# Performance work log

Measured on AMD Instinct MI355X. Metric: run time of the kernel, lower is better.

## Reference

```python
import jax, jax.numpy as jnp
import numpy as np

EPS = 1e-12  # F.normalize default eps

def _unfold3(x):
    # torch F.unfold(kernel=(3,3), padding=1): [B,C,H,W] -> [B, C*9, H*W]
    # channel-major, kernel offsets row-major (matches torch ordering)
    B, C, H, W = x.shape
    xp = jnp.pad(x, ((0, 0), (0, 0), (1, 1), (1, 1)))
    p = jnp.stack([xp[:, :, i:i + H, j:j + W] for i in range(3) for j in range(3)], axis=2)  # [B,C,9,H,W]
    return p.reshape(B, C * 9, H * W)

def _fold3(u, H, W):
    # torch F.fold(output_size=(H,W), kernel=(3,3), padding=1): sums overlapping patches
    B, CK, L = u.shape
    C = CK // 9
    p = u.reshape(B, C, 3, 3, H, W)
    out = jnp.zeros((B, C, H + 2, W + 2), u.dtype)
    for i in range(3):
        for j in range(3):
            out = out.at[:, :, i:i + H, j:j + W].add(p[:, :, i, j])
    return out[:, :, 1:H + 1, 1:W + 1]

def setup_inputs() -> dict:
    key = jax.random.key(0)
    k1, k2, k3 = jax.random.split(key, 3)
    B, C, H, W = 4, 64, 64, 64
    return {
        "lrsr_lv3": jax.random.normal(k1, (B, C, H, W), jnp.float32),
        "refsr_lv3": jax.random.normal(k2, (B, C, H, W), jnp.float32),
        "ref_lv3": jax.random.normal(k3, (B, C, H, W), jnp.float32),
    }

def reference(lrsr_lv3, refsr_lv3, ref_lv3):
    B, C, H, W = lrsr_lv3.shape
    lr_u = _unfold3(lrsr_lv3)                         # [B, D, L_lr], D = C*9
    rs_u = _unfold3(refsr_lv3).transpose(0, 2, 1)     # [B, L_ref, D]
    rs_u = rs_u / jnp.maximum(jnp.linalg.norm(rs_u, axis=2, keepdims=True), EPS)
    lr_u = lr_u / jnp.maximum(jnp.linalg.norm(lr_u, axis=1, keepdims=True), EPS)
    corr = jnp.einsum('brd,bdl->brl', rs_u, lr_u)     # [B, L_ref, L_lr]
    s = jnp.max(corr, axis=1)                         # [B, L_lr]
    arg = jnp.argmax(corr, axis=1)                    # [B, L_lr]
    ref_u = _unfold3(ref_lv3)                         # [B, D, L_ref]
    trans_u = jnp.take_along_axis(ref_u, arg[:, None, :], axis=2)  # [B, D, L_lr]
    trans_lv3 = _fold3(trans_u, H, W)                 # [B, C, H, W]
    return s.reshape(B, 1, H, W), trans_lv3
```

## Files before the change

kernel.cpp:

```cpp
#include <hip/hip_runtime.h>

#define BATCH 4
#define CH    64
#define HH    64
#define WW    64
#define LL    4096
#define SPLITS 4
#define RPS   1024
#define BM    128
#define BN    128
#define NRT   (RPS/BM)

#define RSTB  192
#define BSOFF 24576

#define PAD_L   4356
#define GP_BYTE_BASE 1048576
#define GP_SIDE_STRIDE 6690816
#define GP_B_STRIDE    1672704
#define GP_COMP_STRIDE 557568
#define GP_TOTAL       13381632

#define WS_SSQ_RS 0
#define WS_SSQ_LR 16384
#define WS_INV_RS 32768
#define WS_INV_LR 49152
#define WS_PMAX   65536
#define WS_PARG   131072
#define WS_ARG    196608

typedef __attribute__((ext_vector_type(8))) short short8b;
typedef __attribute__((ext_vector_type(4))) float f32x4;

__device__ __forceinline__ void gload16(const void* g, void* l) {
    __builtin_amdgcn_global_load_lds(
        (const __attribute__((address_space(1))) unsigned int*)g,
        (__attribute__((address_space(3))) unsigned int*)l, 16, 0, 0);
}

__global__ void k_split(const float* __restrict__ lrsr,
                        const float* __restrict__ refsr,
                        float* __restrict__ ws) {
    int tid  = threadIdx.x;
    int pos  = blockIdx.x * 256 + tid;
    int c8   = blockIdx.y;
    int side = blockIdx.z >> 2;
    int b    = blockIdx.z & 3;
    const float* src = (side ? lrsr : refsr) + (size_t)b * CH * LL + c8 * 8 * LL + pos;
    int ppos = (pos >> 6) * 66 + (pos & 63) + 67;
    char* dst = (char*)ws + GP_BYTE_BASE + side * GP_SIDE_STRIDE + b * GP_B_STRIDE
              + (size_t)(c8 * PAD_L + ppos) * 16;
    union { unsigned short u[8]; uint4 v; } w0, w1, w2;
    #pragma unroll
    for (int cc = 0; cc < 8; ++cc) {
        float x = src[cc * LL];
        unsigned u0 = __float_as_uint(x);
        float f0 = __uint_as_float(u0 & 0xffff0000u);
        float r1 = x - f0;
        unsigned u1 = __float_as_uint(r1);
        float f1 = __uint_as_float(u1 & 0xffff0000u);
        float r2 = r1 - f1;
        w0.u[cc] = (unsigned short)(u0 >> 16);
        w1.u[cc] = (unsigned short)(u1 >> 16);
        w2.u[cc] = (unsigned short)(__float_as_uint(r2) >> 16);
    }
    *(uint4*)(dst)                      = w0.v;
    *(uint4*)(dst + GP_COMP_STRIDE)     = w1.v;
    *(uint4*)(dst + 2 * GP_COMP_STRIDE) = w2.v;
}

__global__ void k_ssq(const float* __restrict__ lrsr,
                      const float* __restrict__ refsr,
                      float* __restrict__ ws) {
    int t = blockIdx.x * 256 + threadIdx.x;
    int b = t >> 12;
    int r = t & (LL - 1);
    const float* pl = lrsr + (size_t)b * CH * LL + r;
    const float* pr = refsr + (size_t)b * CH * LL + r;
    float sl = 0.f, sr = 0.f;
    #pragma unroll 8
    for (int c = 0; c < CH; ++c) {
        float a = pl[c * LL]; sl += a * a;
        float d = pr[c * LL]; sr += d * d;
    }
    ws[WS_SSQ_RS + t] = sr;
    ws[WS_SSQ_LR + t] = sl;
}

__global__ void k_inv(float* __restrict__ ws) {
    int t = blockIdx.x * 256 + threadIdx.x;
    int b = t >> 12;
    int r = t & (LL - 1);
    int y = r >> 6, x = r & 63;
    float srs = 0.f, slr = 0.f;
    for (int di = -1; di <= 1; ++di) {
        int yy = y + di;
        if ((unsigned)yy >= (unsigned)HH) continue;
        for (int dj = -1; dj <= 1; ++dj) {
            int xx = x + dj;
            if ((unsigned)xx >= (unsigned)WW) continue;
            int idx = b * LL + yy * WW + xx;
            srs += ws[WS_SSQ_RS + idx];
            slr += ws[WS_SSQ_LR + idx];
        }
    }
    ws[WS_INV_RS + t] = 1.f / fmaxf(sqrtf(srs), 1e-12f);
    ws[WS_INV_LR + t] = 1.f / fmaxf(sqrtf(slr), 1e-12f);
}

__global__ __launch_bounds__(256, 2)
void k_corrmax(float* __restrict__ ws) {
    __shared__ __align__(16) unsigned short LDSB[24576];
    __shared__ float sm[256];
    __shared__ int   si[256];

    int tid  = threadIdx.x;
    int b    = blockIdx.z;
    int l0   = blockIdx.x * BN;
    int rbs  = blockIdx.y * RPS;

    int lane = tid & 63;
    int w    = tid >> 6;
    int wr   = w >> 1;
    int wc   = w & 1;
    int ln   = lane & 15;
    int g    = lane >> 4;

    const float* invn_rs = ws + WS_INV_RS + b * LL;
    const char* gp  = (const char*)ws + GP_BYTE_BASE + b * GP_B_STRIDE;
    const char* bp  = gp + ((w < 2) ? 0 : GP_SIDE_STRIDE);

    int LC[12];
    int LB[12];
    {
        int wm = (w & 1) * 12;
        #pragma unroll
        for (int n = 0; n < 12; ++n) {
            int mm  = wm + n;
            int G   = mm * 64 + lane;
            int row = G / 12;
            int rem = G - row * 12;
            int comp = rem >> 2;
            int sl   = rem & 3;
            int o    = sl ^ ((row >> 2) & 3);
            LC[n] = (comp * (8 * PAD_L) + o * PAD_L + row + 2 * (row >> 6)) * 16;
            LB[n] = ((w < 2) ? 0 : BSOFF) + mm * 1024;
        }
    }

    int arow[4], brow[4];
    int swz = (g ^ ((ln >> 2) & 3)) << 4;
    #pragma unroll
    for (int mf = 0; mf < 4; ++mf) {
        arow[mf] = (wr * 64 + mf * 16 + ln) * RSTB + swz;
        brow[mf] = BSOFF + (wc * 64 + mf * 16 + ln) * RSTB + swz;
    }

    int y0B = l0 >> 6;
    int y0A0 = rbs >> 6;

    auto issue = [&](int rt2, int q2, int h2) {
        int i2 = (q2 < 3) ? -1 : ((q2 < 6) ? 0 : 1);
        int j2 = q2 - (i2 + 1) * 3 - 1;
        int y0 = (w < 2) ? (y0A0 + rt2 * 2) : y0B;
        int su = (h2 * (4 * PAD_L) + (y0 + 1 + i2) * 66 + 1 + j2) * 16;
        #pragma unroll
        for (int n = 0; n < 12; ++n)
            gload16(bp + (su + LC[n]), (char*)LDSB + LB[n]);
    };

    float run_m = -1e30f;
    int   run_a = 0;

    issue(0, 0, 0);
    __syncthreads();

    for (int rt = 0; rt < NRT; ++rt) {
        int r0 = rbs + rt * BM;

        f32x4 acc[4][4];
        #pragma unroll
        for (int mf = 0; mf < 4; ++mf)
            #pragma unroll
            for (int nf = 0; nf < 4; ++nf)
                acc[mf][nf] = (f32x4){0.f, 0.f, 0.f, 0.f};

        for (int q = 0; q < 9; ++q) {
            for (int h = 0; h < 2; ++h) {
                short8b a[4][3], bb[4][3];
                const char* lc = (const char*)LDSB;
                #pragma unroll
                for (int mf = 0; mf < 4; ++mf)
                    #pragma unroll
                    for (int c = 0; c < 3; ++c) {
                        a[mf][c]  = *(const short8b*)(lc + arow[mf] + c * 64);
                        bb[mf][c] = *(const short8b*)(lc + brow[mf] + c * 64);
                    }
                __syncthreads();

                {
                    int h2 = h ^ 1, q2 = q, rt2 = rt;
                    if (h == 1) { q2 = q + 1; h2 = 0; if (q2 == 9) { q2 = 0; rt2 = rt + 1; } }
                    issue(rt2, q2, h2);
                }

                #pragma unroll
                for (int mf = 0; mf < 4; ++mf)
                    #pragma unroll
                    for (int nf = 0; nf < 4; ++nf) {
                        f32x4 d = acc[mf][nf];
                        d = __builtin_amdgcn_mfma_f32_16x16x32_bf16(a[mf][0], bb[nf][0], d, 0, 0, 0);
                        d = __builtin_amdgcn_mfma_f32_16x16x32_bf16(a[mf][0], bb[nf][1], d, 0, 0, 0);
                        d = __builtin_amdgcn_mfma_f32_16x16x32_bf16(a[mf][1], bb[nf][0], d, 0, 0, 0);
                        d = __builtin_amdgcn_mfma_f32_16x16x32_bf16(a[mf][1], bb[nf][1], d, 0, 0, 0);
                        d = __builtin_amdgcn_mfma_f32_16x16x32_bf16(a[mf][0], bb[nf][2], d, 0, 0, 0);
                        d = __builtin_amdgcn_mfma_f32_16x16x32_bf16(a[mf][2], bb[nf][0], d, 0, 0, 0);
                        acc[mf][nf] = d;
                    }
                __syncthreads();
            }
        }

        #pragma unroll
        for (int nf = 0; nf < 4; ++nf) {
            float bv = -1e30f; int bi = 0;
            #pragma unroll
            for (int mf = 0; mf < 4; ++mf) {
                #pragma unroll
                for (int reg = 0; reg < 4; ++reg) {
                    int r = r0 + wr * 64 + mf * 16 + g * 4 + reg;
                    float val = acc[mf][nf][reg] * invn_rs[r];
                    if (val > bv || (val == bv && r < bi)) { bv = val; bi = r; }
                }
            }
            #pragma unroll
            for (int ofs = 16; ofs < 64; ofs <<= 1) {
                float ov = __shfl_xor(bv, ofs);
                int   oi = __shfl_xor(bi, ofs);
                if (ov > bv || (ov == bv && oi < bi)) { bv = ov; bi = oi; }
            }
            if (g == 0) {
                int col = wc * 64 + nf * 16 + ln;
                sm[wr * 128 + col] = bv;
                si[wr * 128 + col] = bi;
            }
        }
        __syncthreads();
        if (tid < 128) {
            float bm = run_m; int ba = run_a;
            #pragma unroll
            for (int ww = 0; ww < 2; ++ww) {
                float v = sm[ww * 128 + tid];
                int   a2 = si[ww * 128 + tid];
                if (v > bm || (v == bm && a2 < ba)) { bm = v; ba = a2; }
            }
            run_m = bm; run_a = ba;
        }
        __syncthreads();
    }

    if (tid < 128) {
        int l = l0 + tid;
        int o = (b * SPLITS + blockIdx.y) * LL + l;
        ws[WS_PMAX + o] = run_m;
        ((int*)ws)[WS_PARG + o] = run_a;
    }
}

__global__ void k_reduce(float* __restrict__ ws, float* __restrict__ out) {
    int t = blockIdx.x * 256 + threadIdx.x;
    int b = t >> 12;
    int l = t & (LL - 1);
    float bm = -1e30f; int ba = 0;
    for (int s = 0; s < SPLITS; ++s) {
        int o = (b * SPLITS + s) * LL + l;
        float v = ws[WS_PMAX + o];
        int   a = ((int*)ws)[WS_PARG + o];
        if (v > bm || (v == bm && a < ba)) { bm = v; ba = a; }
    }
    out[t] = bm * ws[WS_INV_LR + t];
    ((int*)ws)[WS_ARG + t] = ba;
}

__global__ void k_fold(const float* __restrict__ ref,
                       const float* __restrict__ ws,
                       float* __restrict__ out) {
    int t = blockIdx.x * 256 + threadIdx.x;
    int b = t >> 18;
    int c = (t >> 12) & 63;
    int yx = t & (LL - 1);
    int y = yx >> 6, x = yx & 63;
    const int* ab = ((const int*)ws) + WS_ARG + b * LL;
    const float* rb = ref + (size_t)b * CH * LL + c * LL;
    float s = 0.f;
    #pragma unroll
    for (int i = 0; i < 3; ++i) {
        int yp = y + 1 - i;
        if ((unsigned)yp >= (unsigned)HH) continue;
        #pragma unroll
        for (int j = 0; j < 3; ++j) {
            int xp = x + 1 - j;
            if ((unsigned)xp >= (unsigned)WW) continue;
            int r = ab[yp * WW + xp];
            int ry = (r >> 6) + i - 1;
            int rx = (r & 63) + j - 1;
            if ((unsigned)ry < (unsigned)HH && (unsigned)rx < (unsigned)WW)
                s += rb[ry * WW + rx];
        }
    }
    out[BATCH * LL + t] = s;
}

extern "C" void kernel_launch(void* const* d_in, const int* in_sizes, int n_in,
                              void* d_out, int out_size, void* d_ws, size_t ws_size,
                              hipStream_t stream) {
    const float* lrsr = (const float*)d_in[0];
    const float* refsr = (const float*)d_in[1];
    const float* ref  = (const float*)d_in[2];
    float* out = (float*)d_out;
    float* ws  = (float*)d_ws;

    hipMemsetAsync((char*)d_ws + GP_BYTE_BASE, 0, GP_TOTAL, stream);
    k_split<<<dim3(16, 8, 8), dim3(256), 0, stream>>>(lrsr, refsr, ws);
    k_ssq<<<dim3(BATCH * LL / 256), dim3(256), 0, stream>>>(lrsr, refsr, ws);
    k_inv<<<dim3(BATCH * LL / 256), dim3(256), 0, stream>>>(ws);
    k_corrmax<<<dim3(LL / BN, SPLITS, BATCH), dim3(256), 0, stream>>>(ws);
    k_reduce<<<dim3(BATCH * LL / 256), dim3(256), 0, stream>>>(ws, out);
    k_fold<<<dim3(BATCH * CH * LL / 256), dim3(256), 0, stream>>>(ref, ws, out);
}
```

Measured before the change: 425.9 us.

## Double row splits, keep per-wave running max in registers, raise occupancy

```diff
diff --git a/kernel.cpp b/kernel.cpp
--- a/kernel.cpp
+++ b/kernel.cpp
@@ -5,8 +5,8 @@
 #define HH    64
 #define WW    64
 #define LL    4096
-#define SPLITS 4
-#define RPS   1024
+#define SPLITS 8
+#define RPS   512
 #define BM    128
 #define BN    128
 #define NRT   (RPS/BM)
@@ -15,7 +15,7 @@
 #define BSOFF 24576
 
 #define PAD_L   4356
-#define GP_BYTE_BASE 1048576
+#define GP_BYTE_BASE 1376256
 #define GP_SIDE_STRIDE 6690816
 #define GP_B_STRIDE    1672704
 #define GP_COMP_STRIDE 557568
@@ -26,8 +26,8 @@
 #define WS_INV_RS 32768
 #define WS_INV_LR 49152
 #define WS_PMAX   65536
-#define WS_PARG   131072
-#define WS_ARG    196608
+#define WS_PARG   196608
+#define WS_ARG    327680
 
 typedef __attribute__((ext_vector_type(8))) short short8b;
 typedef __attribute__((ext_vector_type(4))) float f32x4;
@@ -108,11 +108,9 @@
     ws[WS_INV_LR + t] = 1.f / fmaxf(sqrtf(slr), 1e-12f);
 }
 
-__global__ __launch_bounds__(256, 2)
+__global__ __launch_bounds__(256, 3)
 void k_corrmax(float* __restrict__ ws) {
     __shared__ __align__(16) unsigned short LDSB[24576];
-    __shared__ float sm[256];
-    __shared__ int   si[256];
 
     int tid  = threadIdx.x;
     int b    = blockIdx.z;
@@ -156,7 +154,7 @@
         brow[mf] = BSOFF + (wc * 64 + mf * 16 + ln) * RSTB + swz;
     }
 
-    int y0B = l0 >> 6;
+    int y0B  = l0 >> 6;
     int y0A0 = rbs >> 6;
 
     auto issue = [&](int rt2, int q2, int h2) {
@@ -169,8 +167,8 @@
             gload16(bp + (su + LC[n]), (char*)LDSB + LB[n]);
     };
 
-    float run_m = -1e30f;
-    int   run_a = 0;
+    float rm[4] = {-1e30f, -1e30f, -1e30f, -1e30f};
+    int   ra[4] = {0, 0, 0, 0};
 
     issue(0, 0, 0);
     __syncthreads();
@@ -204,6 +202,7 @@
                     issue(rt2, q2, h2);
                 }
 
+                __builtin_amdgcn_s_setprio(1);
                 #pragma unroll
                 for (int mf = 0; mf < 4; ++mf)
                     #pragma unroll
@@ -217,10 +216,15 @@
                         d = __builtin_amdgcn_mfma_f32_16x16x32_bf16(a[mf][2], bb[nf][0], d, 0, 0, 0);
                         acc[mf][nf] = d;
                     }
+                __builtin_amdgcn_s_setprio(0);
                 __syncthreads();
             }
         }
 
+        f32x4 inv4[4];
+        #pragma unroll
+        for (int mf = 0; mf < 4; ++mf)
+            inv4[mf] = *(const f32x4*)&invn_rs[r0 + wr * 64 + mf * 16 + g * 4];
         #pragma unroll
         for (int nf = 0; nf < 4; ++nf) {
             float bv = -1e30f; int bi = 0;
@@ -229,7 +233,7 @@
                 #pragma unroll
                 for (int reg = 0; reg < 4; ++reg) {
                     int r = r0 + wr * 64 + mf * 16 + g * 4 + reg;
-                    float val = acc[mf][nf][reg] * invn_rs[r];
+                    float val = acc[mf][nf][reg] * inv4[mf][reg];
                     if (val > bv || (val == bv && r < bi)) { bv = val; bi = r; }
                 }
             }
@@ -239,31 +243,30 @@
                 int   oi = __shfl_xor(bi, ofs);
                 if (ov > bv || (ov == bv && oi < bi)) { bv = ov; bi = oi; }
             }
-            if (g == 0) {
-                int col = wc * 64 + nf * 16 + ln;
-                sm[wr * 128 + col] = bv;
-                si[wr * 128 + col] = bi;
-            }
-        }
-        __syncthreads();
-        if (tid < 128) {
-            float bm = run_m; int ba = run_a;
-            #pragma unroll
-            for (int ww = 0; ww < 2; ++ww) {
-                float v = sm[ww * 128 + tid];
-                int   a2 = si[ww * 128 + tid];
-                if (v > bm || (v == bm && a2 < ba)) { bm = v; ba = a2; }
-            }
-            run_m = bm; run_a = ba;
-        }
-        __syncthreads();
-    }
-
+            if (bv > rm[nf] || (bv == rm[nf] && bi < ra[nf])) { rm[nf] = bv; ra[nf] = bi; }
+        }
+    }
+
+    __syncthreads();
+    float* sm2 = (float*)LDSB;
+    int*   si2 = (int*)LDSB + 256;
+    if (g == 0) {
+        #pragma unroll
+        for (int nf = 0; nf < 4; ++nf) {
+            int col = wc * 64 + nf * 16 + ln;
+            sm2[wr * 128 + col] = rm[nf];
+            si2[wr * 128 + col] = ra[nf];
+        }
+    }
+    __syncthreads();
     if (tid < 128) {
+        float bm = sm2[tid]; int ba = si2[tid];
+        float v  = sm2[128 + tid]; int a2 = si2[128 + tid];
+        if (v > bm || (v == bm && a2 < ba)) { bm = v; ba = a2; }
         int l = l0 + tid;
         int o = (b * SPLITS + blockIdx.y) * LL + l;
-        ws[WS_PMAX + o] = run_m;
-        ((int*)ws)[WS_PARG + o] = run_a;
+        ws[WS_PMAX + o] = bm;
+        ((int*)ws)[WS_PARG + o] = ba;
     }
 }
 
```

Result: slower. 792.2 us (+86.0%).
